# Performance work log

Measured on AMD Instinct MI355X. Metric: run time of the kernel, lower is better.

## Reference

```python
import jax, jax.numpy as jnp
import numpy as np

N_NODES = 100000


def _gcn_norm(edge_index, num_nodes):
    """Add self-loops and compute symmetric GCN normalization coefficients.
    Returns (src, dst, norm) for the augmented edge list."""
    loop = jnp.arange(num_nodes, dtype=edge_index.dtype)
    src = jnp.concatenate([edge_index[0], loop])
    dst = jnp.concatenate([edge_index[1], loop])
    deg = jax.ops.segment_sum(jnp.ones_like(src, dtype=jnp.float32), dst,
                              num_segments=num_nodes)
    dinv = jnp.where(deg > 0, jax.lax.rsqrt(deg), 0.0)
    norm = dinv[src] * dinv[dst]  # [E + N]
    return src, dst, norm


def setup_inputs() -> dict:
    key = jax.random.key(0)
    ks = jax.random.split(key, 7)
    d = 64
    E = 1000000
    x = jax.random.normal(ks[0], (N_NODES, d), dtype=jnp.float32)
    edge_index = jax.random.randint(ks[1], (2, E), 0, N_NODES, dtype=jnp.int64)
    s = 1.0 / np.sqrt(d)
    Ws = jax.random.normal(ks[2], (3, d, d), dtype=jnp.float32) * s
    bs = jax.random.normal(ks[3], (3, d), dtype=jnp.float32) * 0.02
    W_out = jax.random.normal(ks[4], (d, d), dtype=jnp.float32) * s
    b_out = jax.random.normal(ks[5], (d,), dtype=jnp.float32) * 0.02
    return {"x": x, "edge_index": edge_index, "Ws": Ws, "bs": bs,
            "W_out": W_out, "b_out": b_out}


def reference(x, edge_index, Ws, bs, W_out, b_out):
    num_nodes = x.shape[0]
    src, dst, norm = _gcn_norm(edge_index, num_nodes)  # fixed graph -> compute once
    for i in range(Ws.shape[0]):  # small fixed layer count
        h = x @ Ws[i]                              # [N, d] linear transform
        msg = norm[:, None] * h[src]               # gather + scale  [E+N, d]
        x = jax.ops.segment_sum(msg, dst, num_segments=num_nodes) + bs[i]
        x = jax.nn.relu(x)
    return x @ W_out + b_out
```

## Files before the change

### kernel.cpp

```cpp
#include <hip/hip_runtime.h>
#include <hip/hip_bf16.h>

#define D 64
#define BSHIFT 8
#define BNODES 256
#define BCAP 4096
#define PTILE 4096

typedef __attribute__((ext_vector_type(8))) short short8;
typedef __attribute__((ext_vector_type(4))) float float4v;

__device__ __forceinline__ float bf16u_to_f32(unsigned short u) {
  union { unsigned int i; float f; } c;
  c.i = ((unsigned int)u) << 16;
  return c.f;
}

__device__ __forceinline__ unsigned short f32_to_bf16u(float f) {
  union { float f; unsigned int u; } c;
  c.f = f;
  unsigned int r = (c.u + 0x7fffu + ((c.u >> 16) & 1u)) >> 16;
  return (unsigned short)r;
}

__device__ __forceinline__ int wave_f32flag(const void* W) {
  const unsigned short* wb = (const unsigned short*)W;
  int lane = threadIdx.x & 63;
  bool big = false;
  for (int i = lane; i < 512; i += 64) {
    float v = bf16u_to_f32(wb[i]);
    if (!(fabsf(v) < 100.f)) big = true;
  }
  return __any(big) ? 1 : 0;
}
__device__ __forceinline__ int wave_i64flag(const void* ei) {
  const int* e32 = (const int*)ei;
  int lane = threadIdx.x & 63;
  bool nz = (e32[2 * lane + 1] != 0);
  return __any(nz) ? 0 : 1;
}


__global__ __launch_bounds__(256) void k_prep(
    const void* __restrict__ Ws, const void* __restrict__ Wout,
    const void* __restrict__ bs, const void* __restrict__ bout,
    unsigned short* __restrict__ WT, float* __restrict__ biasf,
    int* __restrict__ bucket_cursor) {
  int f32 = wave_f32flag(Ws);
  int gid = blockIdx.x * 256 + threadIdx.x;
  int stride = gridDim.x * 256;

  for (int i = gid; i < 512; i += stride) bucket_cursor[i] = i * BCAP;

  for (int i = gid; i < 4 * 4096; i += stride) {
    int l = i >> 12;
    int r = i & 4095;
    int k = r >> 6;
    int nn = r & 63;
    unsigned short v;
    if (l < 3) {
      v = f32 ? f32_to_bf16u(((const float*)Ws)[l * 4096 + r])
              : ((const unsigned short*)Ws)[l * 4096 + r];
    } else {
      v = f32 ? f32_to_bf16u(((const float*)Wout)[r])
              : ((const unsigned short*)Wout)[r];
    }
    WT[l * 4096 + nn * 64 + k] = v;
  }
  for (int i = gid; i < 4 * 64; i += stride) {
    int l = i >> 6;
    int j = i & 63;
    float v;
    if (l < 3)
      v = f32 ? ((const float*)bs)[l * 64 + j]
              : bf16u_to_f32(((const unsigned short*)bs)[l * 64 + j]);
    else
      v = f32 ? ((const float*)bout)[j]
              : bf16u_to_f32(((const unsigned short*)bout)[j]);
    biasf[i] = v;
  }
}


__global__ __launch_bounds__(256) void k_partition(
    const void* __restrict__ ei, int* __restrict__ bucket_cursor,
    int* __restrict__ packed, int e) {
  __shared__ int lhist[512];
  __shared__ int lbase[512];
  int tid = threadIdx.x;
  int t0 = blockIdx.x * PTILE;
  int tend = min(t0 + PTILE, e);
  if (t0 >= e) return;
  int i64 = wave_i64flag(ei);

  for (int b = tid; b < 512; b += 256) lhist[b] = 0;
  __syncthreads();

  if (i64) {
    const long long* dst = (const long long*)ei + e;
    for (int i = t0 + tid; i < tend; i += 256)
      atomicAdd(&lhist[((int)dst[i]) >> BSHIFT], 1);
  } else {
    const int* dst = (const int*)ei + e;
    for (int i = t0 + tid; i < tend; i += 256)
      atomicAdd(&lhist[dst[i] >> BSHIFT], 1);
  }
  __syncthreads();

  for (int b = tid; b < 512; b += 256) {
    int c = lhist[b];
    lbase[b] = c ? atomicAdd(&bucket_cursor[b], c) : 0;
    lhist[b] = 0;
  }
  __syncthreads();

  if (i64) {
    const long long* srcp = (const long long*)ei;
    const long long* dstp = srcp + e;
    for (int i = t0 + tid; i < tend; i += 256) {
      int s = (int)srcp[i];
      int d = (int)dstp[i];
      int b = d >> BSHIFT;
      int r = atomicAdd(&lhist[b], 1);
      packed[lbase[b] + r] = (s << BSHIFT) | (d & (BNODES - 1));
    }
  } else {
    const int* srcp = (const int*)ei;
    const int* dstp = srcp + e;
    for (int i = t0 + tid; i < tend; i += 256) {
      int s = srcp[i];
      int d = dstp[i];
      int b = d >> BSHIFT;
      int r = atomicAdd(&lhist[b], 1);
      packed[lbase[b] + r] = (s << BSHIFT) | (d & (BNODES - 1));
    }
  }
}

__global__ __launch_bounds__(256) void k_sort_csr(
    const int* __restrict__ packed, const int* __restrict__ bucket_cursor,
    int* __restrict__ csr, int2* __restrict__ rowrange,
    float* __restrict__ dinv, const void* __restrict__ x0,
    const void* __restrict__ Ws, ushort4* __restrict__ za, int n) {
  __shared__ int lcnt[BNODES];
  __shared__ int lofs[BNODES];
  __shared__ int sbuf[BNODES];
  __shared__ float sdinv[BNODES];
  int tid = threadIdx.x;
  int bucket = blockIdx.x;
  int node0 = bucket << BSHIFT;
  int nodes = min(BNODES, n - node0);
  int s0 = bucket * BCAP;
  int s1 = bucket_cursor[bucket];
  lcnt[tid] = 0;
  __syncthreads();
  for (int i = s0 + tid; i < s1; i += 256)
    atomicAdd(&lcnt[packed[i] & (BNODES - 1)], 1);
  __syncthreads();
  int v = lcnt[tid];
  sbuf[tid] = v;
  __syncthreads();
  for (int off = 1; off < BNODES; off <<= 1) {
    int tv = (tid >= off) ? sbuf[tid - off] : 0;
    __syncthreads();
    sbuf[tid] += tv;
    __syncthreads();
  }
  int excl = sbuf[tid] - v;
  lofs[tid] = excl;
  lcnt[tid] = 0;
  float dvv = rsqrtf((float)(v + 1));
  sdinv[tid] = dvv;
  if (tid < nodes) {
    rowrange[node0 + tid] = make_int2(s0 + excl, s0 + excl + v);
    dinv[node0 + tid] = dvv;
  }
  __syncthreads();
  for (int i = s0 + tid; i < s1; i += 256) {
    int pk = packed[i];
    int ld = pk & (BNODES - 1);
    int r = atomicAdd(&lcnt[ld], 1);
    csr[s0 + lofs[ld] + r] = pk >> BSHIFT;
  }

  int f32 = wave_f32flag(Ws);
  int total = nodes * 16;
  for (int i = tid; i < total; i += 256) {
    int r = i >> 4;
    int c4 = i & 15;
    float dv = sdinv[r];
    size_t gi = (size_t)(node0 + r) * 16 + c4;
    ushort4 o;
    if (f32) {
      float4 vv = ((const float4*)x0)[gi];
      o.x = f32_to_bf16u(dv * vv.x);
      o.y = f32_to_bf16u(dv * vv.y);
      o.z = f32_to_bf16u(dv * vv.z);
      o.w = f32_to_bf16u(dv * vv.w);
    } else {
      ushort4 vv = ((const ushort4*)x0)[gi];
      o.x = f32_to_bf16u(dv * bf16u_to_f32(vv.x));
      o.y = f32_to_bf16u(dv * bf16u_to_f32(vv.y));
      o.z = f32_to_bf16u(dv * bf16u_to_f32(vv.z));
      o.w = f32_to_bf16u(dv * bf16u_to_f32(vv.w));
    }
    za[gi] = o;
  }
}

__global__ __launch_bounds__(256, 4) void k_fused(
    const unsigned short* __restrict__ z, const int2* __restrict__ rowrange,
    const int* __restrict__ csr, const float* __restrict__ dinv,
    const unsigned short* __restrict__ WT, const float* __restrict__ biasf,
    unsigned short* __restrict__ out, int n, int scale_out) {
  __shared__ __align__(16) float part[4 * 2048];
  __shared__ unsigned short ybf[16 * 80];
  int tid = threadIdx.x;
  int lane = tid & 63;
  int w = tid >> 6;
  int q = lane >> 4;
  int f = lane & 15;
  int h = lane & 7;
  int g8 = lane >> 3;

  short8 b0 = *(const short8*)(WT + (size_t)(f + 16 * w) * 64 + q * 8);
  short8 b1 = *(const short8*)(WT + (size_t)(f + 16 * w) * 64 + 32 + q * 8);

  int row0 = blockIdx.x * 16;
  int base_node = row0 + w * 4;
  const short8* z8 = (const short8*)z;

  int rrw = 0;
  if (lane < 8) rrw = ((const int*)rowrange)[(size_t)base_node * 2 + lane];
  int rx0 = __shfl(rrw, 0, 64);
  int ry0 = __shfl(rrw, 1, 64);
  int rx1 = __shfl(rrw, 2, 64);
  int ry1 = __shfl(rrw, 3, 64);
  int rx2 = __shfl(rrw, 4, 64);
  int ry2 = __shfl(rrw, 5, 64);
  int rx3 = __shfl(rrw, 6, 64);
  int ry3 = __shfl(rrw, 7, 64);
  int deg0 = ry0 - rx0;
  int deg1 = ry1 - rx1;
  int deg2 = ry2 - rx2;
  int deg3 = ry3 - rx3;

  int jx = lane >> 4;
  int m = lane & 15;
  int rxj = (jx & 2) ? ((jx & 1) ? rx3 : rx2) : ((jx & 1) ? rx1 : rx0);
  int dgj = (jx & 2) ? ((jx & 1) ? deg3 : deg2) : ((jx & 1) ? deg1 : deg0);
  int coff = (m >= 1 && m <= dgj) ? (m - 1) : 0;
  int idx = csr[rxj + coff];
  if (m == 0) idx = base_node + jx;

  float a0[8] = {0, 0, 0, 0, 0, 0, 0, 0};
  float a1[8] = {0, 0, 0, 0, 0, 0, 0, 0};
  float a2[8] = {0, 0, 0, 0, 0, 0, 0, 0};
  float a3[8] = {0, 0, 0, 0, 0, 0, 0, 0};

  short8 g[8];
#pragma unroll
  for (int t = 0; t < 8; t++) {
    int u = ((t & 1) << 3) + g8;
    int sl = ((t >> 1) << 4) + u;
    int s = __shfl(idx, sl, 64);
    g[t] = z8[(size_t)s * 8 + h];
  }
#pragma unroll
  for (int t = 0; t < 8; t++) {
    int u = ((t & 1) << 3) + g8;
    const int j = t >> 1;
    int dg = (j == 0) ? deg0 : (j == 1) ? deg1 : (j == 2) ? deg2 : deg3;
    float vm = (u <= dg) ? 1.f : 0.f;
    float* aj = (j == 0) ? a0 : (j == 1) ? a1 : (j == 2) ? a2 : a3;
#pragma unroll
    for (int c = 0; c < 8; c++)
      aj[c] += vm * bf16u_to_f32((unsigned short)g[t][c]);
  }

#pragma unroll
  for (int j = 0; j < 4; j++) {
    int rx = (j == 0) ? rx0 : (j == 1) ? rx1 : (j == 2) ? rx2 : rx3;
    int dg = (j == 0) ? deg0 : (j == 1) ? deg1 : (j == 2) ? deg2 : deg3;
    float* aj = (j == 0) ? a0 : (j == 1) ? a1 : (j == 2) ? a2 : a3;
    for (int e0 = 15; e0 < dg; e0 += 8) {
      int e = e0 + g8;
      bool vv = e < dg;
      int s = csr[rx + (vv ? e : 0)];
      short8 tv = z8[(size_t)s * 8 + h];
      float vm = vv ? 1.f : 0.f;
#pragma unroll
      for (int c = 0; c < 8; c++)
        aj[c] += vm * bf16u_to_f32((unsigned short)tv[c]);
    }
  }

  char* pb = (char*)part + (w << 13);
  {
    int base_wg = g8 << 8;
#pragma unroll
    for (int j = 0; j < 4; j++) {
      const float* aj = (j == 0) ? a0 : (j == 1) ? a1 : (j == 2) ? a2 : a3;
      int jb = j << 11;
      *(float4*)(pb + jb + base_wg + ((((2 * h) ^ g8)) << 4)) =
          make_float4(aj[0], aj[1], aj[2], aj[3]);
      *(float4*)(pb + jb + base_wg + ((((2 * h + 1) ^ g8)) << 4)) =
          make_float4(aj[4], aj[5], aj[6], aj[7]);
    }
  }
  int jr = lane >> 4;
  int gr = lane & 15;
  float s0 = 0.f, s1 = 0.f, s2 = 0.f, s3 = 0.f;
#pragma unroll
  for (int gg = 0; gg < 8; gg++) {
    float4 v = *(const float4*)(pb + (jr << 11) + (gg << 8) + ((gr ^ gg) << 4));
    s0 += v.x;
    s1 += v.y;
    s2 += v.z;
    s3 += v.w;
  }
  {
    float dv = dinv[base_node + jr];
    unsigned int w0 = (unsigned int)f32_to_bf16u(dv * s0) |
                      ((unsigned int)f32_to_bf16u(dv * s1) << 16);
    unsigned int w1 = (unsigned int)f32_to_bf16u(dv * s2) |
                      ((unsigned int)f32_to_bf16u(dv * s3) << 16);
    *(uint2*)&ybf[(w * 4 + jr) * 80 + 4 * gr] = make_uint2(w0, w1);
  }
  __syncthreads();

  short8 fa0 = *(const short8*)&ybf[f * 80 + q * 8];
  short8 fa1 = *(const short8*)&ybf[f * 80 + 32 + q * 8];
  float4v zz = {0.f, 0.f, 0.f, 0.f};
  float4v acc = __builtin_amdgcn_mfma_f32_16x16x32_bf16(fa0, b0, zz, 0, 0, 0);
  acc = __builtin_amdgcn_mfma_f32_16x16x32_bf16(fa1, b1, acc, 0, 0, 0);

  float bv = biasf[16 * w + f];
  if (scale_out) {
    float4 dv4 = *(const float4*)(dinv + row0 + q * 4);
    float d[4] = {dv4.x, dv4.y, dv4.z, dv4.w};
#pragma unroll
    for (int reg = 0; reg < 4; reg++) {
      int row = row0 + q * 4 + reg;
      if (row < n)
        out[(size_t)row * 64 + 16 * w + f] =
            f32_to_bf16u(d[reg] * fmaxf(acc[reg] + bv, 0.f));
    }
  } else {
#pragma unroll
    for (int reg = 0; reg < 4; reg++) {
      int row = row0 + q * 4 + reg;
      if (row < n)
        out[(size_t)row * 64 + 16 * w + f] =
            f32_to_bf16u(fmaxf(acc[reg] + bv, 0.f));
    }
  }
}

__global__ __launch_bounds__(256) void k_gemm_final(
    const unsigned short* __restrict__ xin,
    const unsigned short* __restrict__ WT, const float* __restrict__ bias,
    void* __restrict__ out, const void* __restrict__ Ws, int ntiles) {
  int lane = threadIdx.x & 63;
  int wid = threadIdx.x >> 6;
  int f = lane & 15;
  int q = lane >> 4;
  int f32o = wave_f32flag(Ws);

  short8 bfr[4][2];
#pragma unroll
  for (int ct = 0; ct < 4; ct++)
#pragma unroll
    for (int kt = 0; kt < 2; kt++)
      bfr[ct][kt] =
          *(const short8*)(WT + (size_t)(f + 16 * ct) * 64 + kt * 32 + q * 8);

  float bv[4];
#pragma unroll
  for (int ct = 0; ct < 4; ct++) bv[ct] = bias[f + 16 * ct];

  int wave = blockIdx.x * 4 + wid;
  int nwaves = gridDim.x * 4;
  for (int t = wave; t < ntiles; t += nwaves) {
    int row0 = t * 16;
    const unsigned short* xr = xin + (size_t)(row0 + f) * 64 + q * 8;
    short8 a0 = *(const short8*)(xr);
    short8 a1 = *(const short8*)(xr + 32);
    float4v acc[4];
#pragma unroll
    for (int ct = 0; ct < 4; ct++) {
      float4v z = {0.f, 0.f, 0.f, 0.f};
      acc[ct] =
          __builtin_amdgcn_mfma_f32_16x16x32_bf16(a0, bfr[ct][0], z, 0, 0, 0);
      acc[ct] = __builtin_amdgcn_mfma_f32_16x16x32_bf16(a1, bfr[ct][1],
                                                        acc[ct], 0, 0, 0);
    }
    if (f32o) {
      float* op = (float*)out;
#pragma unroll
      for (int reg = 0; reg < 4; reg++) {
        size_t rb = (size_t)(row0 + q * 4 + reg) * 64 + f;
#pragma unroll
        for (int ct = 0; ct < 4; ct++) op[rb + 16 * ct] = acc[ct][reg] + bv[ct];
      }
    } else {
      unsigned short* op = (unsigned short*)out;
#pragma unroll
      for (int reg = 0; reg < 4; reg++) {
        size_t rb = (size_t)(row0 + q * 4 + reg) * 64 + f;
#pragma unroll
        for (int ct = 0; ct < 4; ct++)
          op[rb + 16 * ct] = f32_to_bf16u(acc[ct][reg] + bv[ct]);
      }
    }
  }
}


extern "C" void kernel_launch(void* const* d_in, const int* in_sizes, int n_in,
                              void* d_out, int out_size, void* d_ws,
                              size_t ws_size, hipStream_t stream) {
  const void* x0 = d_in[0];
  const void* ei = d_in[1];
  const void* Ws = d_in[2];
  const void* bs = d_in[3];
  const void* Wout = d_in[4];
  const void* bout = d_in[5];

  const int N = in_sizes[0] / D;
  const int E = in_sizes[1] / 2;
  const int NBUC = (N + BNODES - 1) >> BSHIFT;
  const int NT = (N + 15) / 16;

  char* p = (char*)d_ws;
  auto alloc = [&](size_t bytes) {
    char* r = p;
    p += (bytes + 511) & ~(size_t)511;
    return r;
  };
  int* bucket_cursor = (int*)alloc(512 * 4);
  int* packed = (int*)alloc((size_t)512 * BCAP * 4);
  int* csr = (int*)alloc((size_t)512 * BCAP * 4);
  int2* rowrange = (int2*)alloc((size_t)N * 8);
  float* dinv = (float*)alloc((size_t)N * 4);
  unsigned short* WT = (unsigned short*)alloc(4 * 4096 * 2);
  float* biasf = (float*)alloc(4 * 64 * 4);
  unsigned short* za = (unsigned short*)alloc((size_t)N * D * 2);
  unsigned short* zb = (unsigned short*)alloc((size_t)N * D * 2);
  (void)ws_size;
  (void)n_in;
  (void)out_size;

  k_prep<<<32, 256, 0, stream>>>(Ws, Wout, bs, bout, WT, biasf, bucket_cursor);
  int ptiles = (E + PTILE - 1) / PTILE;
  k_partition<<<ptiles, 256, 0, stream>>>(ei, bucket_cursor, packed, E);
  k_sort_csr<<<NBUC, 256, 0, stream>>>(packed, bucket_cursor, csr, rowrange,
                                       dinv, x0, Ws, (ushort4*)za, N);

  k_fused<<<NT, 256, 0, stream>>>(za, rowrange, csr, dinv, WT + 0 * 4096,
                                  biasf + 0 * 64, zb, N, 1);
  k_fused<<<NT, 256, 0, stream>>>(zb, rowrange, csr, dinv, WT + 1 * 4096,
                                  biasf + 1 * 64, za, N, 1);
  k_fused<<<NT, 256, 0, stream>>>(za, rowrange, csr, dinv, WT + 2 * 4096,
                                  biasf + 2 * 64, zb, N, 0);
  k_gemm_final<<<(NT + 3) / 4, 256, 0, stream>>>(zb, WT + 3 * 4096,
                                                 biasf + 3 * 64, d_out, Ws,
                                                 NT);
}
```

Before: 232.1 us.

## Precompute per-tile neighbor slot table to skip rowrange/csr lookups in aggregation

The CSR build kernel now also writes a per-tile slot table holding each node's first 16 neighbor indices (plus the self-loop and a clamped degree), laid out so each lane loads its gather indices with two int4 reads. The fused layer kernels use this table instead of reading rowrange and csr and shuffling indices, and only fall back to the CSR path for nodes with more than 15 neighbors. The degree-scaling of the input moves into a separate grid-stride kernel, and the partition tile size is halved. This trades one extra launch and the table build for fewer dependent loads in each of the three aggregation passes.

```diff
diff --git a/kernel.cpp b/kernel.cpp
--- a/kernel.cpp
+++ b/kernel.cpp
@@ -5,7 +5,7 @@
 #define BSHIFT 8
 #define BNODES 256
 #define BCAP 4096
-#define PTILE 4096
+#define PTILE 2048
 
 typedef __attribute__((ext_vector_type(8))) short short8;
 typedef __attribute__((ext_vector_type(4))) float float4v;
@@ -140,12 +140,10 @@
 __global__ __launch_bounds__(256) void k_sort_csr(
     const int* __restrict__ packed, const int* __restrict__ bucket_cursor,
     int* __restrict__ csr, int2* __restrict__ rowrange,
-    float* __restrict__ dinv, const void* __restrict__ x0,
-    const void* __restrict__ Ws, ushort4* __restrict__ za, int n) {
+    float* __restrict__ dinv, int* __restrict__ slot_tbl, int n) {
   __shared__ int lcnt[BNODES];
   __shared__ int lofs[BNODES];
   __shared__ int sbuf[BNODES];
-  __shared__ float sdinv[BNODES];
   int tid = threadIdx.x;
   int bucket = blockIdx.x;
   int node0 = bucket << BSHIFT;
@@ -170,7 +168,6 @@
   lofs[tid] = excl;
   lcnt[tid] = 0;
   float dvv = rsqrtf((float)(v + 1));
-  sdinv[tid] = dvv;
   if (tid < nodes) {
     rowrange[node0 + tid] = make_int2(s0 + excl, s0 + excl + v);
     dinv[node0 + tid] = dvv;
@@ -182,37 +179,70 @@
     int r = atomicAdd(&lcnt[ld], 1);
     csr[s0 + lofs[ld] + r] = pk >> BSHIFT;
   }
-
+  __syncthreads();
+
+  int node = node0 + tid;
+  int nt16 = ((n + 15) >> 4) << 4;
+  if (node < nt16) {
+    int tile = node >> 4;
+    int w = (node >> 2) & 3;
+    int j = node & 3;
+    int* base = slot_tbl + ((size_t)tile << 8) + (w << 6);
+    if (tid < nodes) {
+      int rx = s0 + excl;
+      int dcl = min(v, 4095);
+#pragma unroll
+      for (int u = 0; u < 16; u++) {
+        int val;
+        if (u == 0)
+          val = node | (dcl << 17);
+        else if (u <= v)
+          val = csr[rx + u - 1];
+        else
+          val = node | (int)0x80000000;
+        base[((u & 7) << 3) + ((j << 1) | (u >> 3))] = val;
+      }
+    } else {
+#pragma unroll
+      for (int u = 0; u < 16; u++)
+        base[((u & 7) << 3) + ((j << 1) | (u >> 3))] = node | (int)0x80000000;
+    }
+  }
+}
+
+
+__global__ __launch_bounds__(256) void k_scale(
+    const void* __restrict__ x0, const void* __restrict__ Ws,
+    const float* __restrict__ dinv, ushort4* __restrict__ z, int n16) {
   int f32 = wave_f32flag(Ws);
-  int total = nodes * 16;
-  for (int i = tid; i < total; i += 256) {
-    int r = i >> 4;
-    int c4 = i & 15;
-    float dv = sdinv[r];
-    size_t gi = (size_t)(node0 + r) * 16 + c4;
+  int i = blockIdx.x * 256 + threadIdx.x;
+  int stride = gridDim.x * 256;
+  for (; i < n16; i += stride) {
+    float d = dinv[i >> 4];
     ushort4 o;
     if (f32) {
-      float4 vv = ((const float4*)x0)[gi];
-      o.x = f32_to_bf16u(dv * vv.x);
-      o.y = f32_to_bf16u(dv * vv.y);
-      o.z = f32_to_bf16u(dv * vv.z);
-      o.w = f32_to_bf16u(dv * vv.w);
+      float4 v = ((const float4*)x0)[i];
+      o.x = f32_to_bf16u(d * v.x);
+      o.y = f32_to_bf16u(d * v.y);
+      o.z = f32_to_bf16u(d * v.z);
+      o.w = f32_to_bf16u(d * v.w);
     } else {
-      ushort4 vv = ((const ushort4*)x0)[gi];
-      o.x = f32_to_bf16u(dv * bf16u_to_f32(vv.x));
-      o.y = f32_to_bf16u(dv * bf16u_to_f32(vv.y));
-      o.z = f32_to_bf16u(dv * bf16u_to_f32(vv.z));
-      o.w = f32_to_bf16u(dv * bf16u_to_f32(vv.w));
-    }
-    za[gi] = o;
+      ushort4 v = ((const ushort4*)x0)[i];
+      o.x = f32_to_bf16u(d * bf16u_to_f32(v.x));
+      o.y = f32_to_bf16u(d * bf16u_to_f32(v.y));
+      o.z = f32_to_bf16u(d * bf16u_to_f32(v.z));
+      o.w = f32_to_bf16u(d * bf16u_to_f32(v.w));
+    }
+    z[i] = o;
   }
 }
 
 __global__ __launch_bounds__(256, 4) void k_fused(
     const unsigned short* __restrict__ z, const int2* __restrict__ rowrange,
     const int* __restrict__ csr, const float* __restrict__ dinv,
-    const unsigned short* __restrict__ WT, const float* __restrict__ biasf,
-    unsigned short* __restrict__ out, int n, int scale_out) {
+    const int* __restrict__ slot_tbl, const unsigned short* __restrict__ WT,
+    const float* __restrict__ biasf, unsigned short* __restrict__ out, int n,
+    int scale_out) {
   __shared__ __align__(16) float part[4 * 2048];
   __shared__ unsigned short ybf[16 * 80];
   int tid = threadIdx.x;
@@ -230,28 +260,11 @@
   int base_node = row0 + w * 4;
   const short8* z8 = (const short8*)z;
 
-  int rrw = 0;
-  if (lane < 8) rrw = ((const int*)rowrange)[(size_t)base_node * 2 + lane];
-  int rx0 = __shfl(rrw, 0, 64);
-  int ry0 = __shfl(rrw, 1, 64);
-  int rx1 = __shfl(rrw, 2, 64);
-  int ry1 = __shfl(rrw, 3, 64);
-  int rx2 = __shfl(rrw, 4, 64);
-  int ry2 = __shfl(rrw, 5, 64);
-  int rx3 = __shfl(rrw, 6, 64);
-  int ry3 = __shfl(rrw, 7, 64);
-  int deg0 = ry0 - rx0;
-  int deg1 = ry1 - rx1;
-  int deg2 = ry2 - rx2;
-  int deg3 = ry3 - rx3;
-
-  int jx = lane >> 4;
-  int m = lane & 15;
-  int rxj = (jx & 2) ? ((jx & 1) ? rx3 : rx2) : ((jx & 1) ? rx1 : rx0);
-  int dgj = (jx & 2) ? ((jx & 1) ? deg3 : deg2) : ((jx & 1) ? deg1 : deg0);
-  int coff = (m >= 1 && m <= dgj) ? (m - 1) : 0;
-  int idx = csr[rxj + coff];
-  if (m == 0) idx = base_node + jx;
+  const int4* tb =
+      (const int4*)(slot_tbl + ((size_t)blockIdx.x << 8) + (w << 6) + (g8 << 3));
+  int4 sA = tb[0];
+  int4 sB = tb[1];
+  int sidx[8] = {sA.x, sA.y, sA.z, sA.w, sB.x, sB.y, sB.z, sB.w};
 
   float a0[8] = {0, 0, 0, 0, 0, 0, 0, 0};
   float a1[8] = {0, 0, 0, 0, 0, 0, 0, 0};
@@ -260,38 +273,52 @@
 
   short8 g[8];
 #pragma unroll
+  for (int t = 0; t < 8; t++)
+    g[t] = z8[(size_t)(sidx[t] & 0x1FFFF) * 8 + h];
+#pragma unroll
   for (int t = 0; t < 8; t++) {
-    int u = ((t & 1) << 3) + g8;
-    int sl = ((t >> 1) << 4) + u;
-    int s = __shfl(idx, sl, 64);
-    g[t] = z8[(size_t)s * 8 + h];
-  }
-#pragma unroll
-  for (int t = 0; t < 8; t++) {
-    int u = ((t & 1) << 3) + g8;
     const int j = t >> 1;
-    int dg = (j == 0) ? deg0 : (j == 1) ? deg1 : (j == 2) ? deg2 : deg3;
-    float vm = (u <= dg) ? 1.f : 0.f;
+    float vm = (sidx[t] >= 0) ? 1.f : 0.f;
     float* aj = (j == 0) ? a0 : (j == 1) ? a1 : (j == 2) ? a2 : a3;
 #pragma unroll
     for (int c = 0; c < 8; c++)
       aj[c] += vm * bf16u_to_f32((unsigned short)g[t][c]);
   }
 
-#pragma unroll
-  for (int j = 0; j < 4; j++) {
-    int rx = (j == 0) ? rx0 : (j == 1) ? rx1 : (j == 2) ? rx2 : rx3;
-    int dg = (j == 0) ? deg0 : (j == 1) ? deg1 : (j == 2) ? deg2 : deg3;
-    float* aj = (j == 0) ? a0 : (j == 1) ? a1 : (j == 2) ? a2 : a3;
-    for (int e0 = 15; e0 < dg; e0 += 8) {
-      int e = e0 + g8;
-      bool vv = e < dg;
-      int s = csr[rx + (vv ? e : 0)];
-      short8 tv = z8[(size_t)s * 8 + h];
-      float vm = vv ? 1.f : 0.f;
-#pragma unroll
-      for (int c = 0; c < 8; c++)
-        aj[c] += vm * bf16u_to_f32((unsigned short)tv[c]);
+  int dg0 = (__shfl(sidx[0], 0, 64) >> 17) & 0xFFF;
+  int dg1 = (__shfl(sidx[2], 0, 64) >> 17) & 0xFFF;
+  int dg2 = (__shfl(sidx[4], 0, 64) >> 17) & 0xFFF;
+  int dg3 = (__shfl(sidx[6], 0, 64) >> 17) & 0xFFF;
+  if (dg0 > 15 || dg1 > 15 || dg2 > 15 || dg3 > 15) {
+    int rrw = 0;
+    if (lane < 8) rrw = ((const int*)rowrange)[(size_t)base_node * 2 + lane];
+    int rx0 = __shfl(rrw, 0, 64);
+    int ry0 = __shfl(rrw, 1, 64);
+    int rx1 = __shfl(rrw, 2, 64);
+    int ry1 = __shfl(rrw, 3, 64);
+    int rx2 = __shfl(rrw, 4, 64);
+    int ry2 = __shfl(rrw, 5, 64);
+    int rx3 = __shfl(rrw, 6, 64);
+    int ry3 = __shfl(rrw, 7, 64);
+    int deg0 = ry0 - rx0;
+    int deg1 = ry1 - rx1;
+    int deg2 = ry2 - rx2;
+    int deg3 = ry3 - rx3;
+#pragma unroll
+    for (int j = 0; j < 4; j++) {
+      int rx = (j == 0) ? rx0 : (j == 1) ? rx1 : (j == 2) ? rx2 : rx3;
+      int dg = (j == 0) ? deg0 : (j == 1) ? deg1 : (j == 2) ? deg2 : deg3;
+      float* aj = (j == 0) ? a0 : (j == 1) ? a1 : (j == 2) ? a2 : a3;
+      for (int e0 = 15; e0 < dg; e0 += 8) {
+        int e = e0 + g8;
+        bool vv = e < dg;
+        int s = csr[rx + (vv ? e : 0)];
+        short8 tv = z8[(size_t)s * 8 + h];
+        float vm = vv ? 1.f : 0.f;
+#pragma unroll
+        for (int c = 0; c < 8; c++)
+          aj[c] += vm * bf16u_to_f32((unsigned short)tv[c]);
+      }
     }
   }
 
@@ -443,6 +470,7 @@
   int* csr = (int*)alloc((size_t)512 * BCAP * 4);
   int2* rowrange = (int2*)alloc((size_t)N * 8);
   float* dinv = (float*)alloc((size_t)N * 4);
+  int* slot_tbl = (int*)alloc((size_t)NT * 256 * 4);
   unsigned short* WT = (unsigned short*)alloc(4 * 4096 * 2);
   float* biasf = (float*)alloc(4 * 64 * 4);
   unsigned short* za = (unsigned short*)alloc((size_t)N * D * 2);
@@ -455,14 +483,15 @@
   int ptiles = (E + PTILE - 1) / PTILE;
   k_partition<<<ptiles, 256, 0, stream>>>(ei, bucket_cursor, packed, E);
   k_sort_csr<<<NBUC, 256, 0, stream>>>(packed, bucket_cursor, csr, rowrange,
-                                       dinv, x0, Ws, (ushort4*)za, N);
-
-  k_fused<<<NT, 256, 0, stream>>>(za, rowrange, csr, dinv, WT + 0 * 4096,
-                                  biasf + 0 * 64, zb, N, 1);
-  k_fused<<<NT, 256, 0, stream>>>(zb, rowrange, csr, dinv, WT + 1 * 4096,
-                                  biasf + 1 * 64, za, N, 1);
-  k_fused<<<NT, 256, 0, stream>>>(za, rowrange, csr, dinv, WT + 2 * 4096,
-                                  biasf + 2 * 64, zb, N, 0);
+                                       dinv, slot_tbl, N);
+  k_scale<<<1024, 256, 0, stream>>>(x0, Ws, dinv, (ushort4*)za, N * 16);
+
+  k_fused<<<NT, 256, 0, stream>>>(za, rowrange, csr, dinv, slot_tbl,
+                                  WT + 0 * 4096, biasf + 0 * 64, zb, N, 1);
+  k_fused<<<NT, 256, 0, stream>>>(zb, rowrange, csr, dinv, slot_tbl,
+                                  WT + 1 * 4096, biasf + 1 * 64, za, N, 1);
+  k_fused<<<NT, 256, 0, stream>>>(za, rowrange, csr, dinv, slot_tbl,
+                                  WT + 2 * 4096, biasf + 2 * 64, zb, N, 0);
   k_gemm_final<<<(NT + 3) / 4, 256, 0, stream>>>(zb, WT + 3 * 4096,
                                                  biasf + 3 * 64, d_out, Ws,
                                                  NT);
```

Measured after the change: 233.0 us. About the same (+0.4%).
